# Performance work log

Hardware: AMD Instinct MI355X
Metric: run time of the kernel (lower is better)

## Reference

```python
import jax, jax.numpy as jnp
import numpy as np

T, B, D, H = 32, 128, 256, 768
MAX_PONDER = 8
EPS = 0.01


def setup_inputs() -> dict:
    key = jax.random.key(0)
    ks = jax.random.split(key, 6)
    s = 1.0 / np.sqrt(H)
    return {
        "input_": jax.random.normal(ks[0], (T, B, D), jnp.float32),
        "W_ih": jax.random.uniform(ks[1], (H, D + 1), jnp.float32, -s, s),
        "W_hh": jax.random.uniform(ks[2], (H, H), jnp.float32, -s, s),
        "b_ih": jax.random.uniform(ks[3], (H,), jnp.float32, -s, s),
        "b_hh": jax.random.uniform(ks[4], (H,), jnp.float32, -s, s),
        "w_p": jax.random.uniform(ks[5], (H,), jnp.float32, -s, s),
        "b_p": jnp.ones((1,), jnp.float32),  # torch reset_parameters fills ponder bias with 1
    }


def reference(input_, W_ih, W_hh, b_ih, b_hh, w_p, b_p):
    T_, B_, D_ = input_.shape
    H_ = W_hh.shape[0]
    dt = input_.dtype
    hx0 = jnp.zeros((B_, H_), dt)

    def time_step(carry, x_t):
        hx, pcost = carry

        def ponder(c, _):
            hx_i, ah, ahx, sc, spc, mask, flag = c
            # input row with ponder flag (0 on first act step, 1 afterwards)
            x_in = jnp.concatenate([x_t, jnp.full((B_, 1), flag, dt)], axis=1)
            # ponder cost assigned for active rows before update
            spc = jnp.where(mask, -ah, spc)
            hx_new = jnp.tanh(x_in @ W_ih.T + b_ih + hx_i @ W_hh.T + b_hh)
            hx_i = jnp.where(mask[:, None], hx_new, hx_i)
            mf = mask.astype(dt)
            ahx = ahx + mf[:, None] * hx_new  # accum_hx += hx (as in source)
            h = jax.nn.sigmoid(hx_new @ w_p + b_p[0])
            ah2 = ah + mf * h
            p = h - jnp.maximum(ah2 - 1.0, 0.0)
            ahx = ahx + (mf * p)[:, None] * hx_new  # accum_hx += p*hx
            sc = sc + mf
            mask2 = ah2 < (1.0 - EPS)
            return (hx_i, ah2, ahx, sc, spc, mask2, jnp.ones((), dt)), None

        init = (hx,
                jnp.zeros((B_,), dt),           # accum_h
                jnp.zeros((B_, H_), dt),        # accum_hx
                jnp.zeros((B_,), dt),           # step_count
                jnp.zeros((B_,), dt),           # step_ponder_cost
                jnp.ones((B_,), bool),          # selector
                jnp.zeros((), dt))              # flag
        (hx_i, ah, ahx, sc, spc, mask, flag), _ = jax.lax.scan(
            ponder, init, None, length=MAX_PONDER)
        hx_out = ahx / sc[:, None]
        return (hx_out, pcost + spc), (hx_out, sc)

    (hx_last, pcost), (all_hx, steps) = jax.lax.scan(
        time_step, (hx0, jnp.zeros((B_,), dt)), input_)
    # all_hx: [T,B,H], hx: [1,B,H], ponder_cost: [B], ponder_times: [T,B]
    return all_hx, hx_last[None], pcost, steps
```

## Files before the change

kernel.cpp:

```cpp
#include <hip/hip_runtime.h>
#include <math.h>

#define TT 32
#define BB 128
#define DD 256
#define HH 768
#define MAXP 8

#define RG   8
#define RPG  16
#define CB   12
#define CS   64
#define NTH  256
#define NCH  24
#define NBUF 4

#define OFF_LAST  ((size_t)TT * BB * HH)
#define OFF_PCOST (OFF_LAST + (size_t)BB * HH)
#define OFF_STEPS (OFF_PCOST + BB)

#define ASCOPE __HIP_MEMORY_SCOPE_AGENT
#define SENT   0xFFFFFFFFFFFFFFFFull

typedef __attribute__((ext_vector_type(8))) short s16x8;
typedef __attribute__((ext_vector_type(4))) float f32x4;
typedef unsigned long long ull;

static __device__ __forceinline__ unsigned short f2bf(float f) {
    unsigned u = __float_as_uint(f);
    u = (u + 0x7fffu + ((u >> 16) & 1u)) >> 16;
    return (unsigned short)u;
}
static __device__ __forceinline__ float bf2f(unsigned short h) {
    return __uint_as_float(((unsigned)h) << 16);
}
static __device__ __forceinline__ float fast_tanh(float v) {
    return 1.f - 2.f / (__expf(2.f * v) + 1.f);
}

__launch_bounds__(NTH, 1)
__global__ void act_kernel(const float* __restrict__ x,
                           const float* __restrict__ Wih,
                           const float* __restrict__ Whh,
                           const float* __restrict__ bih,
                           const float* __restrict__ bhh,
                           const float* __restrict__ wpv,
                           const float* __restrict__ bp,
                           float* __restrict__ out,
                           ull* __restrict__ hxe,
                           float* __restrict__ zpt)
{
    const int tid  = threadIdx.x;
    const int rg   = blockIdx.x & 7;
    const int cbk  = blockIdx.x >> 3;
    const int r0   = rg * RPG;
    const int c0   = cbk * CS;
    const int CT   = tid >> 6;
    const int lane = tid & 63;
    const int am   = lane & 15;
    const int aq   = lane >> 4;

    const int pchd  = tid >> 7;
    const int pl    = (tid & 127) >> 1;
    const int phalf = tid & 1;
    const int prow  = pl & 15;
    const int pcol  = pchd*32 + (pl >> 4)*8 + phalf*4;
    const size_t pword = ((size_t)(2*cbk + pchd)*64 + pl)*2 + phalf;

    __shared__ s16x8 A_s[NCH * 64];
    __shared__ s16x8 WB_s[4 * 8 * 64];
    __shared__ s16x8 xA_s[8 * 64];
    __shared__ __align__(16) unsigned short hxn_s[RPG][72];
    __shared__ float wp_s[CS];

    s16x8 Breg[NCH];
    {
        const float* wr = Whh + (size_t)(c0 + CT*16 + am) * HH + aq*8;
        for (int ch = 0; ch < NCH; ++ch) {
            float4 a0 = *(const float4*)(wr + ch*32);
            float4 a1 = *(const float4*)(wr + ch*32 + 4);
            union { s16x8 v; unsigned short e[8]; } u;
            u.e[0]=f2bf(a0.x); u.e[1]=f2bf(a0.y); u.e[2]=f2bf(a0.z); u.e[3]=f2bf(a0.w);
            u.e[4]=f2bf(a1.x); u.e[5]=f2bf(a1.y); u.e[6]=f2bf(a1.z); u.e[7]=f2bf(a1.w);
            Breg[ch] = u.v;
        }
    }
    for (int ch = 0; ch < 8; ++ch) {
        const float* wr = Wih + (size_t)(c0 + CT*16 + am) * (DD+1) + ch*32 + aq*8;
        union { s16x8 v; unsigned short e[8]; } u;
        #pragma unroll
        for (int j = 0; j < 8; ++j) u.e[j] = f2bf(wr[j]);
        WB_s[(CT*8 + ch)*64 + lane] = u.v;
    }
    if (tid < CS) wp_s[tid] = wpv[c0 + tid];
    const int myc = c0 + CT*16 + am;
    const float bs_lane = bih[myc] + bhh[myc];
    const float wfl     = Wih[(size_t)myc*(DD+1) + DD];
    const float bp0     = bp[0];
    {
        s16x8 z8 = {0,0,0,0,0,0,0,0};
        #pragma unroll
        for (int j = 0; j < 6; ++j) A_s[j*NTH + tid] = z8;
    }

    float pc = 0.f;
    unsigned it = 0;

    auto publish = [&]() {
        const unsigned par = it & (NBUF-1);
        ull*   exw = hxe + (size_t)(rg*NBUF + par) * (NCH*64*2);
        float* zpw = zpt + (size_t)(rg*NBUF + par) * (RPG*CB);
        __hip_atomic_store(exw + pword, *(const ull*)&hxn_s[prow][pcol],
                           __ATOMIC_RELAXED, ASCOPE);
        if (CT == 0) {
            const int zr = lane >> 2, zc = lane & 3;
            float sz = 0.f;
            #pragma unroll
            for (int i = 0; i < 16; ++i)
                sz += bf2f(hxn_s[zr][zc*16 + i]) * wp_s[zc*16 + i];
            sz += __shfl_xor(sz, 1);
            sz += __shfl_xor(sz, 2);
            if (zc == 0)
                __hip_atomic_store(&zpw[zr*CB + cbk], sz, __ATOMIC_RELAXED, ASCOPE);
        }
        ++it;
    };

    for (int t = 0; t < TT; ++t) {
        #pragma unroll
        for (int j = 0; j < 2; ++j) {
            const int s = j*NTH + tid;
            const int ch = s >> 6;
            const float* xb = x + ((size_t)t*BB + r0 + am)*DD + ch*32 + aq*8;
            float4 a0 = *(const float4*)xb;
            float4 a1 = *(const float4*)(xb + 4);
            union { s16x8 v; unsigned short e[8]; } u;
            u.e[0]=f2bf(a0.x); u.e[1]=f2bf(a0.y); u.e[2]=f2bf(a0.z); u.e[3]=f2bf(a0.w);
            u.e[4]=f2bf(a1.x); u.e[5]=f2bf(a1.y); u.e[6]=f2bf(a1.z); u.e[7]=f2bf(a1.w);
            xA_s[s] = u.v;
        }
        __syncthreads();

        f32x4 xi;
        {
            f32x4 a = {0.f,0.f,0.f,0.f};
            #pragma unroll
            for (int ch = 0; ch < 8; ++ch)
                a = __builtin_amdgcn_mfma_f32_16x16x32_bf16(
                        xA_s[ch*64 + lane], WB_s[(CT*8 + ch)*64 + lane], a, 0, 0, 0);
            xi[0]=a[0]+bs_lane; xi[1]=a[1]+bs_lane; xi[2]=a[2]+bs_lane; xi[3]=a[3]+bs_lane;
        }

        float ahx[48];
        #pragma unroll
        for (int q = 0; q < 48; ++q) ahx[q] = 0.f;
        float ah = 0.f, sc = 0.f, spc = 0.f;
        int act = 1;

        {
            f32x4 acc = xi;
            #pragma unroll
            for (int ch = 0; ch < NCH; ++ch)
                acc = __builtin_amdgcn_mfma_f32_16x16x32_bf16(
                        A_s[ch*64 + lane], Breg[ch], acc, 0, 0, 0);
            #pragma unroll
            for (int r = 0; r < 4; ++r)
                hxn_s[aq*4 + r][CT*16 + am] = f2bf(fast_tanh(acc[r]));
        }
        __syncthreads();
        publish();

        for (int pk = 1; ; ++pk) {
            const unsigned rpar = (it - 1u) & (NBUF-1);
            const ull* exr = hxe + (size_t)(rg*NBUF + rpar) * (NCH*64*2);
            const ull* zbr = (const ull*)(zpt + (size_t)(rg*NBUF + rpar) * (RPG*CB) + am*CB);

            ull hv[12], zv[6];
            unsigned hok = 0, zok = 0;
            for (;;) {
                #pragma unroll
                for (int j = 0; j < 6; ++j) {
                    const ull* src = exr + ((size_t)((j*4 + CT)*64 + lane))*2;
                    if (!(hok & (1u << (2*j)))) {
                        hv[2*j] = __hip_atomic_load(src, __ATOMIC_RELAXED, ASCOPE);
                        if (hv[2*j] != SENT) hok |= 1u << (2*j);
                    }
                    if (!(hok & (1u << (2*j+1)))) {
                        hv[2*j+1] = __hip_atomic_load(src+1, __ATOMIC_RELAXED, ASCOPE);
                        if (hv[2*j+1] != SENT) hok |= 1u << (2*j+1);
                    }
                }
                #pragma unroll
                for (int j = 0; j < 6; ++j) {
                    if (!(zok & (1u << j))) {
                        zv[j] = __hip_atomic_load(zbr + j, __ATOMIC_RELAXED, ASCOPE);
                        if ((unsigned)(zv[j] & 0xffffffffu) != 0xffffffffu &&
                            (unsigned)(zv[j] >> 32)         != 0xffffffffu)
                            zok |= 1u << j;
                    }
                }
                if (__all((int)(hok == 0xfffu && zok == 0x3fu))) break;
            }

            {
                const unsigned cpar = (it + 1u) & (NBUF-1);
                ull*   exc = hxe + (size_t)(rg*NBUF + cpar) * (NCH*64*2);
                float* zpc = zpt + (size_t)(rg*NBUF + cpar) * (RPG*CB);
                __hip_atomic_store(exc + pword, SENT, __ATOMIC_RELAXED, ASCOPE);
                if (tid < RPG)
                    __hip_atomic_store(&zpc[tid*CB + cbk],
                                       __uint_as_float(0xffffffffu),
                                       __ATOMIC_RELAXED, ASCOPE);
            }

            #pragma unroll
            for (int j = 0; j < 6; ++j) {
                union { ull u[2]; s16x8 v; } cv;
                cv.u[0] = hv[2*j]; cv.u[1] = hv[2*j+1];
                A_s[(j*4 + CT)*64 + lane] = cv.v;
            }

            float zf[12];
            #pragma unroll
            for (int j = 0; j < 6; ++j) {
                zf[2*j]   = __uint_as_float((unsigned)(zv[j] & 0xffffffffu));
                zf[2*j+1] = __uint_as_float((unsigned)(zv[j] >> 32));
            }
            const float zA = (zf[0]+zf[1]) + (zf[2]+zf[3]);
            const float zB = (zf[4]+zf[5]) + (zf[6]+zf[7]);
            const float zC = (zf[8]+zf[9]) + (zf[10]+zf[11]);
            const float z  = (zA + zB) + zC;
            const float h  = 1.f / (1.f + __expf(-(z + bp0)));
            float w1 = 0.f;
            if (act) {
                spc = -ah;
                ah += h;
                w1 = 1.f + (h - fmaxf(ah - 1.f, 0.f));
                sc += 1.f;
                act = (ah < 0.99f) ? 1 : 0;
            }
            const bool done = __all(act == 0) || (pk == MAXP);

            if (done) {
                #pragma unroll
                for (int j = 0; j < 6; ++j) {
                    #pragma unroll
                    for (int i = 0; i < 4; ++i) {
                        ahx[j*8 + i]     += w1 * bf2f((unsigned short)(hv[2*j]   >> (16*i)));
                        ahx[j*8 + 4 + i] += w1 * bf2f((unsigned short)(hv[2*j+1] >> (16*i)));
                    }
                }
                break;
            }
            __syncthreads();

            f32x4 acc = xi;
            #pragma unroll
            for (int ch = 0; ch < NCH; ++ch)
                acc = __builtin_amdgcn_mfma_f32_16x16x32_bf16(
                        A_s[ch*64 + lane], Breg[ch], acc, 0, 0, 0);
            #pragma unroll
            for (int j = 0; j < 6; ++j) {
                #pragma unroll
                for (int i = 0; i < 4; ++i) {
                    ahx[j*8 + i]     += w1 * bf2f((unsigned short)(hv[2*j]   >> (16*i)));
                    ahx[j*8 + 4 + i] += w1 * bf2f((unsigned short)(hv[2*j+1] >> (16*i)));
                }
            }
            #pragma unroll
            for (int r = 0; r < 4; ++r)
                hxn_s[aq*4 + r][CT*16 + am] = f2bf(fast_tanh(acc[r] + wfl));
            __syncthreads();
            publish();
        }

        const float inv = 1.f / sc;
        pc += spc;
        if (cbk == 0 && tid < RPG) out[OFF_STEPS + (size_t)t*BB + r0 + tid] = sc;
        #pragma unroll
        for (int j = 0; j < 6; ++j) {
            const int ch = j*4 + CT;
            float o[8];
            #pragma unroll
            for (int i = 0; i < 8; ++i) o[i] = ahx[j*8 + i] * inv;
            union { s16x8 v; unsigned short e[8]; } u;
            #pragma unroll
            for (int i = 0; i < 8; ++i) u.e[i] = f2bf(o[i]);
            A_s[ch*64 + lane] = u.v;
            if (cbk == 0) {
                float* op = out + ((size_t)t*BB + r0 + am)*HH + ch*32 + aq*8;
                *(float4*)op       = make_float4(o[0], o[1], o[2], o[3]);
                *(float4*)(op + 4) = make_float4(o[4], o[5], o[6], o[7]);
                if (t == TT-1) {
                    float* lp = out + OFF_LAST + (size_t)(r0 + am)*HH + ch*32 + aq*8;
                    *(float4*)lp       = make_float4(o[0], o[1], o[2], o[3]);
                    *(float4*)(lp + 4) = make_float4(o[4], o[5], o[6], o[7]);
                }
            }
        }
    }
    if (cbk == 0 && tid < RPG) out[OFF_PCOST + r0 + tid] = pc;
}

extern "C" void kernel_launch(void* const* d_in, const int* in_sizes, int n_in,
                              void* d_out, int out_size, void* d_ws, size_t ws_size,
                              hipStream_t stream) {
    const float* x   = (const float*)d_in[0];
    const float* Wih = (const float*)d_in[1];
    const float* Whh = (const float*)d_in[2];
    const float* bih = (const float*)d_in[3];
    const float* bhh = (const float*)d_in[4];
    const float* wpv = (const float*)d_in[5];
    const float* bp  = (const float*)d_in[6];
    float* out = (float*)d_out;

    ull*   hxe = (ull*)d_ws;
    float* zpt = (float*)((char*)d_ws + (size_t)RG*NBUF*NCH*64*16);

    hipMemsetAsync(d_ws, 0xFF, (size_t)RG*NBUF*NCH*64*16 + (size_t)RG*NBUF*RPG*CB*4,
                   stream);
    act_kernel<<<dim3(RG*CB), dim3(NTH), 0, stream>>>(
        x, Wih, Whh, bih, bhh, wpv, bp, out, hxe, zpt);
}
```

Baseline: 437.0 us.

## Add per-block progress flags to gate exchange polling and move sentinel reset into publish

Adds a per-block progress counter array. One wave polls the 12 counters of its row group before any thread reads the exchanged hidden-state chunks, so all 256 threads no longer spin on data sentinels. Publishing now happens from a single wave with wider stores, and the sentinel reset for the buffer two steps ahead moves into publish. The cost is an extra flag round trip and a __syncthreads per ponder step. The sentinel check on the data is still kept.

```diff
diff --git a/kernel.cpp b/kernel.cpp
--- a/kernel.cpp
+++ b/kernel.cpp
@@ -47,6 +47,7 @@
                            const float* __restrict__ wpv,
                            const float* __restrict__ bp,
                            float* __restrict__ out,
+                           unsigned* __restrict__ flags,
                            ull* __restrict__ hxe,
                            float* __restrict__ zpt)
 {
@@ -63,8 +64,6 @@
     const int pchd  = tid >> 7;
     const int pl    = (tid & 127) >> 1;
     const int phalf = tid & 1;
-    const int prow  = pl & 15;
-    const int pcol  = pchd*32 + (pl >> 4)*8 + phalf*4;
     const size_t pword = ((size_t)(2*cbk + pchd)*64 + pl)*2 + phalf;
 
     __shared__ s16x8 A_s[NCH * 64];
@@ -108,11 +107,19 @@
 
     auto publish = [&]() {
         const unsigned par = it & (NBUF-1);
-        ull*   exw = hxe + (size_t)(rg*NBUF + par) * (NCH*64*2);
-        float* zpw = zpt + (size_t)(rg*NBUF + par) * (RPG*CB);
-        __hip_atomic_store(exw + pword, *(const ull*)&hxn_s[prow][pcol],
-                           __ATOMIC_RELAXED, ASCOPE);
         if (CT == 0) {
+            ull*   exw = hxe + (size_t)(rg*NBUF + par) * (NCH*64*2);
+            float* zpw = zpt + (size_t)(rg*NBUF + par) * (RPG*CB);
+            const ull s00 = ((const ull*)&hxn_s[am][aq*8])[0];
+            const ull s01 = ((const ull*)&hxn_s[am][aq*8])[1];
+            const ull s10 = ((const ull*)&hxn_s[am][32 + aq*8])[0];
+            const ull s11 = ((const ull*)&hxn_s[am][32 + aq*8])[1];
+            ull* d0 = exw + ((size_t)(2*cbk)*64   + lane)*2;
+            ull* d1 = exw + ((size_t)(2*cbk+1)*64 + lane)*2;
+            __hip_atomic_store(d0,   s00, __ATOMIC_RELAXED, ASCOPE);
+            __hip_atomic_store(d0+1, s01, __ATOMIC_RELAXED, ASCOPE);
+            __hip_atomic_store(d1,   s10, __ATOMIC_RELAXED, ASCOPE);
+            __hip_atomic_store(d1+1, s11, __ATOMIC_RELAXED, ASCOPE);
             const int zr = lane >> 2, zc = lane & 3;
             float sz = 0.f;
             #pragma unroll
@@ -122,8 +129,19 @@
             sz += __shfl_xor(sz, 2);
             if (zc == 0)
                 __hip_atomic_store(&zpw[zr*CB + cbk], sz, __ATOMIC_RELAXED, ASCOPE);
+            if (lane == 0)
+                __hip_atomic_store(&flags[rg*16 + cbk], it + 1u, __ATOMIC_RELAXED, ASCOPE);
         }
         ++it;
+        {
+            const unsigned cpar = (it + 1u) & (NBUF-1);
+            ull*   exc = hxe + (size_t)(rg*NBUF + cpar) * (NCH*64*2);
+            float* zpc = zpt + (size_t)(rg*NBUF + cpar) * (RPG*CB);
+            __hip_atomic_store(exc + pword, SENT, __ATOMIC_RELAXED, ASCOPE);
+            if (tid < RPG)
+                __hip_atomic_store((unsigned*)&zpc[tid*CB + cbk], 0xffffffffu,
+                                   __ATOMIC_RELAXED, ASCOPE);
+        }
     };
 
     for (int t = 0; t < TT; ++t) {
@@ -171,60 +189,57 @@
         publish();
 
         for (int pk = 1; ; ++pk) {
-            const unsigned rpar = (it - 1u) & (NBUF-1);
-            const ull* exr = hxe + (size_t)(rg*NBUF + rpar) * (NCH*64*2);
-            const ull* zbr = (const ull*)(zpt + (size_t)(rg*NBUF + rpar) * (RPG*CB) + am*CB);
-
-            ull hv[12], zv[6];
+            if (CT == 0) {
+                const int pi = lane % 12;
+                unsigned v;
+                do { v = __hip_atomic_load(&flags[rg*16 + pi], __ATOMIC_RELAXED, ASCOPE); }
+                while (!__all((int)(v >= it)));
+            }
+            __syncthreads();
+
+            const unsigned parR = (it - 1u) & (NBUF-1);
+            const ull* exr = hxe + (size_t)(rg*NBUF + parR) * (NCH*64*2);
+            const ull* zb  = (const ull*)(zpt + (size_t)(rg*NBUF + parR) * (RPG*CB) + am*CB);
+
+            ull clo[6], chi[6], zu[6];
             unsigned hok = 0, zok = 0;
             for (;;) {
                 #pragma unroll
                 for (int j = 0; j < 6; ++j) {
                     const ull* src = exr + ((size_t)((j*4 + CT)*64 + lane))*2;
                     if (!(hok & (1u << (2*j)))) {
-                        hv[2*j] = __hip_atomic_load(src, __ATOMIC_RELAXED, ASCOPE);
-                        if (hv[2*j] != SENT) hok |= 1u << (2*j);
+                        clo[j] = __hip_atomic_load(src, __ATOMIC_RELAXED, ASCOPE);
+                        if (clo[j] != SENT) hok |= 1u << (2*j);
                     }
                     if (!(hok & (1u << (2*j+1)))) {
-                        hv[2*j+1] = __hip_atomic_load(src+1, __ATOMIC_RELAXED, ASCOPE);
-                        if (hv[2*j+1] != SENT) hok |= 1u << (2*j+1);
+                        chi[j] = __hip_atomic_load(src+1, __ATOMIC_RELAXED, ASCOPE);
+                        if (chi[j] != SENT) hok |= 1u << (2*j+1);
                     }
                 }
                 #pragma unroll
                 for (int j = 0; j < 6; ++j) {
                     if (!(zok & (1u << j))) {
-                        zv[j] = __hip_atomic_load(zbr + j, __ATOMIC_RELAXED, ASCOPE);
-                        if ((unsigned)(zv[j] & 0xffffffffu) != 0xffffffffu &&
-                            (unsigned)(zv[j] >> 32)         != 0xffffffffu)
+                        zu[j] = __hip_atomic_load(zb + j, __ATOMIC_RELAXED, ASCOPE);
+                        if ((unsigned)(zu[j] & 0xffffffffu) != 0xffffffffu &&
+                            (unsigned)(zu[j] >> 32)         != 0xffffffffu)
                             zok |= 1u << j;
                     }
                 }
                 if (__all((int)(hok == 0xfffu && zok == 0x3fu))) break;
             }
 
-            {
-                const unsigned cpar = (it + 1u) & (NBUF-1);
-                ull*   exc = hxe + (size_t)(rg*NBUF + cpar) * (NCH*64*2);
-                float* zpc = zpt + (size_t)(rg*NBUF + cpar) * (RPG*CB);
-                __hip_atomic_store(exc + pword, SENT, __ATOMIC_RELAXED, ASCOPE);
-                if (tid < RPG)
-                    __hip_atomic_store(&zpc[tid*CB + cbk],
-                                       __uint_as_float(0xffffffffu),
-                                       __ATOMIC_RELAXED, ASCOPE);
-            }
-
             #pragma unroll
             for (int j = 0; j < 6; ++j) {
                 union { ull u[2]; s16x8 v; } cv;
-                cv.u[0] = hv[2*j]; cv.u[1] = hv[2*j+1];
+                cv.u[0] = clo[j]; cv.u[1] = chi[j];
                 A_s[(j*4 + CT)*64 + lane] = cv.v;
             }
 
             float zf[12];
             #pragma unroll
             for (int j = 0; j < 6; ++j) {
-                zf[2*j]   = __uint_as_float((unsigned)(zv[j] & 0xffffffffu));
-                zf[2*j+1] = __uint_as_float((unsigned)(zv[j] >> 32));
+                zf[2*j]   = __uint_as_float((unsigned)(zu[j] & 0xffffffffu));
+                zf[2*j+1] = __uint_as_float((unsigned)(zu[j] >> 32));
             }
             const float zA = (zf[0]+zf[1]) + (zf[2]+zf[3]);
             const float zB = (zf[4]+zf[5]) + (zf[6]+zf[7]);
@@ -246,8 +261,8 @@
                 for (int j = 0; j < 6; ++j) {
                     #pragma unroll
                     for (int i = 0; i < 4; ++i) {
-                        ahx[j*8 + i]     += w1 * bf2f((unsigned short)(hv[2*j]   >> (16*i)));
-                        ahx[j*8 + 4 + i] += w1 * bf2f((unsigned short)(hv[2*j+1] >> (16*i)));
+                        ahx[j*8 + i]     += w1 * bf2f((unsigned short)(clo[j] >> (16*i)));
+                        ahx[j*8 + 4 + i] += w1 * bf2f((unsigned short)(chi[j] >> (16*i)));
                     }
                 }
                 break;
@@ -263,8 +278,8 @@
             for (int j = 0; j < 6; ++j) {
                 #pragma unroll
                 for (int i = 0; i < 4; ++i) {
-                    ahx[j*8 + i]     += w1 * bf2f((unsigned short)(hv[2*j]   >> (16*i)));
-                    ahx[j*8 + 4 + i] += w1 * bf2f((unsigned short)(hv[2*j+1] >> (16*i)));
+                    ahx[j*8 + i]     += w1 * bf2f((unsigned short)(clo[j] >> (16*i)));
+                    ahx[j*8 + 4 + i] += w1 * bf2f((unsigned short)(chi[j] >> (16*i)));
                 }
             }
             #pragma unroll
@@ -314,11 +329,13 @@
     const float* bp  = (const float*)d_in[6];
     float* out = (float*)d_out;
 
-    ull*   hxe = (ull*)d_ws;
-    float* zpt = (float*)((char*)d_ws + (size_t)RG*NBUF*NCH*64*16);
-
-    hipMemsetAsync(d_ws, 0xFF, (size_t)RG*NBUF*NCH*64*16 + (size_t)RG*NBUF*RPG*CB*4,
-                   stream);
+    unsigned* flags = (unsigned*)d_ws;
+    ull*      hxe   = (ull*)((char*)d_ws + 4096);
+    float*    zpt   = (float*)((char*)d_ws + 4096 + (size_t)RG*NBUF*NCH*64*16);
+
+    hipMemsetAsync(d_ws, 0, 4096, stream);
+    hipMemsetAsync((char*)d_ws + 4096, 0xFF,
+                   (size_t)RG*NBUF*NCH*64*16 + (size_t)RG*NBUF*RPG*CB*4, stream);
     act_kernel<<<dim3(RG*CB), dim3(NTH), 0, stream>>>(
-        x, Wih, Whh, bih, bhh, wpv, bp, out, hxe, zpt);
-}
+        x, Wih, Whh, bih, bhh, wpv, bp, out, flags, hxe, zpt);
+}
```

After: 486.0 us. +11.2%, slower.
